# Kernel optimization log

Measured on AMD Instinct MI355X. Metric: run time of the kernel, lower is better.

## Reference

```python
import jax, jax.numpy as jnp
import numpy as np

SLOT_DIM = 256
HIDDEN = 128
NUM_REL = 8


def setup_inputs() -> dict:
    key = jax.random.key(0)
    ks = jax.random.split(key, 5)
    B, N, D = 8, 256, SLOT_DIM
    slots = jax.random.normal(ks[0], (B, N, D), dtype=jnp.float32)
    # Linear(2D -> H): store as [2D, H] (x @ W + b)
    s1 = 1.0 / np.sqrt(2 * D)
    W1 = jax.random.uniform(ks[1], (2 * D, HIDDEN), jnp.float32, -s1, s1)
    b1 = jax.random.uniform(ks[2], (HIDDEN,), jnp.float32, -s1, s1)
    s2 = 1.0 / np.sqrt(HIDDEN)
    W2 = jax.random.uniform(ks[3], (HIDDEN, NUM_REL), jnp.float32, -s2, s2)
    b2 = jax.random.uniform(ks[4], (NUM_REL,), jnp.float32, -s2, s2)
    return {"slots": slots, "W1": W1, "b1": b1, "W2": W2, "b2": b2}


def reference(slots, W1, b1, W2, b2):
    # cat([slots_i, slots_j]) @ W1 == slots_i @ W1[:D] + slots_j @ W1[D:]
    # so project each slot once, then broadcast-add over the pair grid.
    D = slots.shape[-1]
    proj_i = jnp.einsum("bnd,dh->bnh", slots, W1[:D])   # [B,N,H]
    proj_j = jnp.einsum("bnd,dh->bnh", slots, W1[D:])   # [B,N,H]
    h = proj_i[:, :, None, :] + proj_j[:, None, :, :] + b1  # [B,N,N,H]
    h = jax.nn.relu(h)
    logits = jnp.einsum("bijh,hr->bijr", h, W2) + b2     # [B,N,N,R]
    return jax.nn.sigmoid(logits)
```

## Files before the change

kernel.cpp:

```cpp
#include <hip/hip_runtime.h>
#include <math.h>

#define BATCH 8
#define NSLOT 256
#define DDIM  256
#define HID   128
#define NREL  8

__global__ __launch_bounds__(256, 2) void proj_kernel(
    const float* __restrict__ slots, const float* __restrict__ W1,
    const float* __restrict__ b1, float* __restrict__ P) {
  const int tid  = threadIdx.x;
  const int row0 = blockIdx.x * 4;
  const int c    = tid;
  const bool isP1 = (c < HID);
  const float* Wcol = isP1 ? (W1 + c) : (W1 + DDIM * HID + (c - HID));
  const float bias = isP1 ? b1[c] : 0.0f;

  float acc[4];
#pragma unroll
  for (int r = 0; r < 4; ++r) acc[r] = bias;

  const float* srow = slots + (size_t)row0 * DDIM;

  for (int k = 0; k < DDIM; k += 16) {
    float w[16];
#pragma unroll
    for (int u = 0; u < 16; ++u) w[u] = Wcol[(size_t)(k + u) * HID];
#pragma unroll
    for (int u = 0; u < 16; ++u) {
#pragma unroll
      for (int r = 0; r < 4; ++r) {
        acc[r] = fmaf(srow[r * DDIM + k + u], w[u], acc[r]);
      }
    }
  }

#pragma unroll
  for (int r = 0; r < 4; ++r) {
    P[(size_t)(row0 + r) * 256 + c] = acc[r];
  }
}

__global__ __launch_bounds__(256, 8) void pair_kernel(
    const float* __restrict__ P, const float* __restrict__ W2,
    const float* __restrict__ b2, float* __restrict__ out) {
  __shared__ float4 Pi4[16 * 33];
  __shared__ float4 Pj4[16 * 33];

  const int tid = threadIdx.x;
  const int j0  = blockIdx.x * 16;
  const int i0  = blockIdx.y * 16;
  const int b   = blockIdx.z;
  const float* Pb = P + (size_t)b * NSLOT * 256;

  {
    const int r  = tid >> 5;
    const int c4 = tid & 31;
    Pi4[(r)     * 33 + c4] = *(const float4*)&Pb[(size_t)(i0 + r)     * 256 + c4 * 4];
    Pi4[(r + 8) * 33 + c4] = *(const float4*)&Pb[(size_t)(i0 + r + 8) * 256 + c4 * 4];
    Pj4[(r)     * 33 + c4] = *(const float4*)&Pb[(size_t)(j0 + r)     * 256 + 128 + c4 * 4];
    Pj4[(r + 8) * 33 + c4] = *(const float4*)&Pb[(size_t)(j0 + r + 8) * 256 + 128 + c4 * 4];
  }
  __syncthreads();

  const int tj = tid & 15;
  const int ti = tid >> 4;

  float acc[NREL];
#pragma unroll
  for (int r = 0; r < NREL; ++r) acc[r] = 0.0f;

#pragma unroll 2
  for (int kc = 0; kc < 32; ++kc) {
    const float4 a = Pi4[ti * 33 + kc];
    const float4 c = Pj4[tj * 33 + kc];
    float h[4];
    h[0] = fmaxf(a.x + c.x, 0.0f);
    h[1] = fmaxf(a.y + c.y, 0.0f);
    h[2] = fmaxf(a.z + c.z, 0.0f);
    h[3] = fmaxf(a.w + c.w, 0.0f);
#pragma unroll
    for (int kk = 0; kk < 4; ++kk) {
      const int k = kc * 4 + kk;
#pragma unroll
      for (int r = 0; r < NREL; ++r) {
        acc[r] = fmaf(h[kk], W2[k * NREL + r], acc[r]);
      }
    }
  }

  float res[8] __attribute__((aligned(16)));
#pragma unroll
  for (int r = 0; r < NREL; ++r) {
    const float x = acc[r] + b2[r];
    res[r] = 1.0f / (1.0f + __expf(-x));
  }
  float* o = out + (((size_t)b * NSLOT + (i0 + ti)) * NSLOT + (j0 + tj)) * NREL;
  *(float4*)&o[0] = *(const float4*)&res[0];
  *(float4*)&o[4] = *(const float4*)&res[4];
}

extern "C" void kernel_launch(void* const* d_in, const int* in_sizes, int n_in,
                              void* d_out, int out_size, void* d_ws, size_t ws_size,
                              hipStream_t stream) {
  const float* slots = (const float*)d_in[0];
  const float* W1    = (const float*)d_in[1];
  const float* b1    = (const float*)d_in[2];
  const float* W2    = (const float*)d_in[3];
  const float* b2    = (const float*)d_in[4];
  float* out = (float*)d_out;
  float* P   = (float*)d_ws;

  proj_kernel<<<dim3(BATCH * NSLOT / 4), 256, 0, stream>>>(slots, W1, b1, P);
  pair_kernel<<<dim3(NSLOT / 16, NSLOT / 16, BATCH), 256, 0, stream>>>(P, W2, b2, out);
}
```

Baseline: 95.89 us.

## Store projections in fp16 and compute pair MLP with MFMA f16 instructions

The projection kernel now writes fp16 projections and processes two rows per block instead of four. The pair kernel computes the relu(Pi+Pj) hidden vectors in packed fp16 and does the 128x8 second-layer matmul with 16x16x32 f16 MFMA instructions, padding the 8 relations to 16. Each wave keeps its j-row projections in registers while the block stages the i-rows in shared memory. This replaces scalar FP32 FMAs with matrix-core work and halves intermediate traffic, at the cost of fp16 precision in the hidden activations and half of the MFMA output being wasted.

```diff
diff --git a/kernel.cpp b/kernel.cpp
--- a/kernel.cpp
+++ b/kernel.cpp
@@ -1,4 +1,5 @@
 #include <hip/hip_runtime.h>
+#include <hip/hip_fp16.h>
 #include <math.h>
 
 #define BATCH 8
@@ -7,20 +8,27 @@
 #define HID   128
 #define NREL  8
 
-__global__ __launch_bounds__(256, 2) void proj_kernel(
+typedef _Float16 half8 __attribute__((ext_vector_type(8)));
+typedef float float4v __attribute__((ext_vector_type(4)));
+
+union U8 {
+  uint32_t u[4];
+  _Float16 f[8];
+  half8 v;
+  float4 f4;
+};
+
+__global__ __launch_bounds__(256, 4) void proj_kernel(
     const float* __restrict__ slots, const float* __restrict__ W1,
-    const float* __restrict__ b1, float* __restrict__ P) {
+    const float* __restrict__ b1, _Float16* __restrict__ P) {
   const int tid  = threadIdx.x;
-  const int row0 = blockIdx.x * 4;
+  const int row0 = blockIdx.x * 2;
   const int c    = tid;
   const bool isP1 = (c < HID);
   const float* Wcol = isP1 ? (W1 + c) : (W1 + DDIM * HID + (c - HID));
   const float bias = isP1 ? b1[c] : 0.0f;
 
-  float acc[4];
-#pragma unroll
-  for (int r = 0; r < 4; ++r) acc[r] = bias;
-
+  float acc0 = bias, acc1 = bias;
   const float* srow = slots + (size_t)row0 * DDIM;
 
   for (int k = 0; k < DDIM; k += 16) {
@@ -29,76 +37,76 @@
     for (int u = 0; u < 16; ++u) w[u] = Wcol[(size_t)(k + u) * HID];
 #pragma unroll
     for (int u = 0; u < 16; ++u) {
+      acc0 = fmaf(srow[k + u], w[u], acc0);
+      acc1 = fmaf(srow[DDIM + k + u], w[u], acc1);
+    }
+  }
+
+  P[(size_t)(row0)     * 256 + c] = (_Float16)acc0;
+  P[(size_t)(row0 + 1) * 256 + c] = (_Float16)acc1;
+}
+
+__global__ __launch_bounds__(256) void pair_kernel(
+    const _Float16* __restrict__ P, const float* __restrict__ W2,
+    const float* __restrict__ b2, float* __restrict__ out) {
+  __shared__ uint32_t PiL[16 * 68];
+
+  const int tid  = threadIdx.x;
+  const int w    = tid >> 6;
+  const int lane = tid & 63;
+  const int n    = lane & 15;
+  const int kg   = lane >> 4;
+
+  const int b   = blockIdx.z;
+  const int i0  = blockIdx.y * 16;
+  const int j0  = blockIdx.x * 64 + w * 16;
+  const _Float16* Pb = P + (size_t)b * NSLOT * 256;
+
+  {
+    const int r  = tid >> 4;
+    const int ch = tid & 15;
+    const float4 t = *(const float4*)(Pb + (size_t)(i0 + r) * 256 + ch * 8);
+    *(float4*)&PiL[r * 68 + ch * 4] = t;
+  }
+  __syncthreads();
+
+  U8 w2f[4];
 #pragma unroll
-      for (int r = 0; r < 4; ++r) {
-        acc[r] = fmaf(srow[r * DDIM + k + u], w[u], acc[r]);
+  for (int kq = 0; kq < 4; ++kq) {
+#pragma unroll
+    for (int u = 0; u < 8; ++u) {
+      const int k = kq * 32 + kg * 8 + u;
+      w2f[kq].f[u] = (n < 8) ? (_Float16)W2[k * NREL + n] : (_Float16)0.0f;
+    }
+  }
+  const float b2v = (n < 8) ? b2[n] : 0.0f;
+
+  U8 pj[4];
+#pragma unroll
+  for (int kq = 0; kq < 4; ++kq) {
+    pj[kq].f4 = *(const float4*)(Pb + (size_t)(j0 + n) * 256 + HID + kq * 32 + kg * 8);
+  }
+
+  for (int i = 0; i < 16; ++i) {
+    float4v acc = {0.0f, 0.0f, 0.0f, 0.0f};
+#pragma unroll
+    for (int kq = 0; kq < 4; ++kq) {
+      U8 pi;
+      pi.f4 = *(const float4*)&PiL[i * 68 + kq * 16 + kg * 4];
+      U8 h;
+      h.v = __builtin_elementwise_max(pj[kq].v + pi.v, (half8)(_Float16)0.0f);
+      acc = __builtin_amdgcn_mfma_f32_16x16x32_f16(h.v, w2f[kq].v, acc, 0, 0, 0);
+    }
+    if (n < 8) {
+      float* obase = out + (((size_t)b * NSLOT + (i0 + i)) * NSLOT + j0) * NREL + n;
+#pragma unroll
+      for (int reg = 0; reg < 4; ++reg) {
+        const int jrow = kg * 4 + reg;
+        const float x = acc[reg] + b2v;
+        obase[jrow * NREL] = __builtin_amdgcn_rcpf(1.0f + __expf(-x));
       }
     }
   }
-
-#pragma unroll
-  for (int r = 0; r < 4; ++r) {
-    P[(size_t)(row0 + r) * 256 + c] = acc[r];
-  }
-}
-
-__global__ __launch_bounds__(256, 8) void pair_kernel(
-    const float* __restrict__ P, const float* __restrict__ W2,
-    const float* __restrict__ b2, float* __restrict__ out) {
-  __shared__ float4 Pi4[16 * 33];
-  __shared__ float4 Pj4[16 * 33];
-
-  const int tid = threadIdx.x;
-  const int j0  = blockIdx.x * 16;
-  const int i0  = blockIdx.y * 16;
-  const int b   = blockIdx.z;
-  const float* Pb = P + (size_t)b * NSLOT * 256;
-
-  {
-    const int r  = tid >> 5;
-    const int c4 = tid & 31;
-    Pi4[(r)     * 33 + c4] = *(const float4*)&Pb[(size_t)(i0 + r)     * 256 + c4 * 4];
-    Pi4[(r + 8) * 33 + c4] = *(const float4*)&Pb[(size_t)(i0 + r + 8) * 256 + c4 * 4];
-    Pj4[(r)     * 33 + c4] = *(const float4*)&Pb[(size_t)(j0 + r)     * 256 + 128 + c4 * 4];
-    Pj4[(r + 8) * 33 + c4] = *(const float4*)&Pb[(size_t)(j0 + r + 8) * 256 + 128 + c4 * 4];
-  }
-  __syncthreads();
-
-  const int tj = tid & 15;
-  const int ti = tid >> 4;
-
-  float acc[NREL];
-#pragma unroll
-  for (int r = 0; r < NREL; ++r) acc[r] = 0.0f;
-
-#pragma unroll 2
-  for (int kc = 0; kc < 32; ++kc) {
-    const float4 a = Pi4[ti * 33 + kc];
-    const float4 c = Pj4[tj * 33 + kc];
-    float h[4];
-    h[0] = fmaxf(a.x + c.x, 0.0f);
-    h[1] = fmaxf(a.y + c.y, 0.0f);
-    h[2] = fmaxf(a.z + c.z, 0.0f);
-    h[3] = fmaxf(a.w + c.w, 0.0f);
-#pragma unroll
-    for (int kk = 0; kk < 4; ++kk) {
-      const int k = kc * 4 + kk;
-#pragma unroll
-      for (int r = 0; r < NREL; ++r) {
-        acc[r] = fmaf(h[kk], W2[k * NREL + r], acc[r]);
-      }
-    }
-  }
-
-  float res[8] __attribute__((aligned(16)));
-#pragma unroll
-  for (int r = 0; r < NREL; ++r) {
-    const float x = acc[r] + b2[r];
-    res[r] = 1.0f / (1.0f + __expf(-x));
-  }
-  float* o = out + (((size_t)b * NSLOT + (i0 + ti)) * NSLOT + (j0 + tj)) * NREL;
-  *(float4*)&o[0] = *(const float4*)&res[0];
-  *(float4*)&o[4] = *(const float4*)&res[4];
 }
 
 extern "C" void kernel_launch(void* const* d_in, const int* in_sizes, int n_in,
@@ -109,9 +117,9 @@
   const float* b1    = (const float*)d_in[2];
   const float* W2    = (const float*)d_in[3];
   const float* b2    = (const float*)d_in[4];
-  float* out = (float*)d_out;
-  float* P   = (float*)d_ws;
+  float* out    = (float*)d_out;
+  _Float16* P   = (_Float16*)d_ws;
 
-  proj_kernel<<<dim3(BATCH * NSLOT / 4), 256, 0, stream>>>(slots, W1, b1, P);
-  pair_kernel<<<dim3(NSLOT / 16, NSLOT / 16, BATCH), 256, 0, stream>>>(P, W2, b2, out);
+  proj_kernel<<<dim3(BATCH * NSLOT / 2), 256, 0, stream>>>(slots, W1, b1, P);
+  pair_kernel<<<dim3(NSLOT / 64, NSLOT / 16, BATCH), 256, 0, stream>>>(P, W2, b2, out);
 }
```

Measured after the change: 86.51 us. 1.11x faster.
